# Performance work log

Hardware: AMD Instinct MI355X
Metric: run time of the kernel (lower is better)

Reference implementation:

```python
import jax, jax.numpy as jnp
import numpy as np

K, B, C, T, D, H = 4, 1024, 128, 64, 64, 4  # timeframes, batch, in-feat, seq(=embed!), embed, heads
HD = D // H
EPS = 1e-5


def setup_inputs() -> dict:
    key = jax.random.key(0)
    ks = jax.random.split(key, 8)
    s = lambda k, shape: jax.random.normal(k, shape, dtype=jnp.float32) * 0.05
    return {
        "feats": jax.random.normal(ks[0], (K, B, C, T), dtype=jnp.float32),
        "proj_w": s(ks[1], (K, D, C)),
        "proj_b": jnp.zeros((K, D), jnp.float32),
        "wq": s(ks[2], (K, D, D)),
        "wk": s(ks[3], (K, D, D)),
        "wv": s(ks[4], (K, D, D)),
        "bq": jnp.zeros((K, D), jnp.float32),
        "bk": jnp.zeros((K, D), jnp.float32),
        "bv": jnp.zeros((K, D), jnp.float32),
        "wo": s(ks[5], (K, D, D)),
        "bo": jnp.zeros((K, D), jnp.float32),
        "ng": jnp.ones((K, D), jnp.float32),
        "nb": jnp.zeros((K, D), jnp.float32),
        "tfw": jnp.full((K,), 1.0 / K, jnp.float32),
        "fg": jnp.ones((K * D,), jnp.float32),
        "fb": jnp.zeros((K * D,), jnp.float32),
    }


def _ln(x, g, b):
    m = x.mean(-1, keepdims=True)
    v = ((x - m) ** 2).mean(-1, keepdims=True)
    return (x - m) * jax.lax.rsqrt(v + EPS) * g + b


def reference(feats, proj_w, proj_b, wq, wk, wv, bq, bk, bv, wo, bo, ng, nb, tfw, fg, fb):
    # per-timeframe Linear on channel axis: [K,B,C,T] -> [K,B,D,T]
    proj = jnp.einsum('kbct,kdc->kbdt', feats, proj_w) + proj_b[:, None, :, None]
    ctx4 = jnp.transpose(proj, (1, 0, 2, 3))              # [B,K,D,T] (torch.stack dim=1)
    ctx = ctx4.reshape(B * D, K, T)                       # replicates torch .view(B*T,K,D); needs T==D
    N = B * D
    scale = 1.0 / np.sqrt(HD)
    outs = []
    for i in range(K):  # small fixed loop over K=4 distinct attention blocks
        q_in = ctx[:, i]                                  # [N,D] query = i-th row
        q = (q_in @ wq[i].T + bq[i]).reshape(N, H, HD)
        k = (ctx @ wk[i].T + bk[i]).reshape(N, K, H, HD)
        v = (ctx @ wv[i].T + bv[i]).reshape(N, K, H, HD)
        sc = jnp.einsum('nhe,nkhe->nhk', q, k) * scale    # [N,H,K]
        a = jax.nn.softmax(sc, axis=-1)
        o = jnp.einsum('nhk,nkhe->nhe', a, v).reshape(N, D)
        o = o @ wo[i].T + bo[i]
        outs.append(_ln(o + q_in, ng[i], nb[i]))          # residual + per-tf LayerNorm
    w = jax.nn.softmax(tfw)
    comb = jnp.stack(outs, axis=1) * w[None, :, None]     # [N,K,D] weighted fusion
    fused = comb.reshape(B, D, K * D)                     # torch .view(B,T,K*D)
    return _ln(fused, fg, fb)
```

## Files before the change

kernel.cpp:

```cpp
#include <hip/hip_runtime.h>
#include <math.h>

#define EPSV 1e-5f

typedef __attribute__((ext_vector_type(8))) short short8;
typedef __attribute__((ext_vector_type(4))) float float4v;

__device__ __forceinline__ unsigned short f2bf(float f) {
  unsigned int x = __float_as_uint(f);
  return (unsigned short)((x + 0x7fffu + ((x >> 16) & 1u)) >> 16);
}
__device__ __forceinline__ float bf2f(unsigned short u) {
  return __uint_as_float(((unsigned int)u) << 16);
}
__device__ __forceinline__ float wave_sum64(float v) {
  v += __shfl_xor(v, 1);
  v += __shfl_xor(v, 2);
  v += __shfl_xor(v, 4);
  v += __shfl_xor(v, 8);
  v += __shfl_xor(v, 16);
  v += __shfl_xor(v, 32);
  return v;
}
__device__ __forceinline__ float group16_sum(float v) {
  v += __shfl_xor(v, 1);
  v += __shfl_xor(v, 2);
  v += __shfl_xor(v, 4);
  v += __shfl_xor(v, 8);
  return v;
}

__global__ __launch_bounds__(256, 2) void proj_kernel(
    const float* __restrict__ feats, const float* __restrict__ pw,
    const float* __restrict__ pb, float* __restrict__ ctx) {
  int kb = blockIdx.x;
  int k = kb >> 10;
  int b = kb & 1023;

  __shared__ __align__(16) float F[128 * 64];
  __shared__ float W[64 * 129];

  const float* fsrc = feats + (size_t)kb * 8192;
  const float* wsrc = pw + k * 8192;
  for (int idx = threadIdx.x; idx < 8192; idx += 256) {
    F[idx] = fsrc[idx];
    W[(idx >> 7) * 129 + (idx & 127)] = wsrc[idx];
  }
  __syncthreads();

  int t4 = threadIdx.x & 15;
  int d4 = threadIdx.x >> 4;

  float pb0 = pb[k * 64 + d4 * 4 + 0];
  float pb1 = pb[k * 64 + d4 * 4 + 1];
  float pb2 = pb[k * 64 + d4 * 4 + 2];
  float pb3 = pb[k * 64 + d4 * 4 + 3];

  float acc[4][4];
#pragma unroll
  for (int j = 0; j < 4; ++j) {
    acc[0][j] = pb0; acc[1][j] = pb1; acc[2][j] = pb2; acc[3][j] = pb3;
  }

#pragma unroll 8
  for (int c = 0; c < 128; ++c) {
    float4 f = *(const float4*)&F[c * 64 + t4 * 4];
    float w0 = W[(d4 * 4 + 0) * 129 + c];
    float w1 = W[(d4 * 4 + 1) * 129 + c];
    float w2 = W[(d4 * 4 + 2) * 129 + c];
    float w3 = W[(d4 * 4 + 3) * 129 + c];
    acc[0][0] += w0 * f.x; acc[0][1] += w0 * f.y; acc[0][2] += w0 * f.z; acc[0][3] += w0 * f.w;
    acc[1][0] += w1 * f.x; acc[1][1] += w1 * f.y; acc[1][2] += w1 * f.z; acc[1][3] += w1 * f.w;
    acc[2][0] += w2 * f.x; acc[2][1] += w2 * f.y; acc[2][2] += w2 * f.z; acc[2][3] += w2 * f.w;
    acc[3][0] += w3 * f.x; acc[3][1] += w3 * f.y; acc[3][2] += w3 * f.z; acc[3][3] += w3 * f.w;
  }

  size_t base = ((size_t)b * 64 + k * 16 + d4) * 256 + t4 * 4;
#pragma unroll
  for (int r = 0; r < 4; ++r) {
    float4 o;
    o.x = acc[r][0]; o.y = acc[r][1]; o.z = acc[r][2]; o.w = acc[r][3];
    *(float4*)&ctx[base + r * 64] = o;
  }
}

__global__ __launch_bounds__(256, 2) void attn_fused(
    const float* __restrict__ ctx32,
    const float* __restrict__ wq, const float* __restrict__ wk,
    const float* __restrict__ wv, const float* __restrict__ wo,
    const float* __restrict__ bq, const float* __restrict__ bk,
    const float* __restrict__ bv, const float* __restrict__ bo,
    const float* __restrict__ ng, const float* __restrict__ nb,
    const float* __restrict__ tfw, float* __restrict__ out) {
  __shared__ __align__(16) unsigned short CTP[64 * 264];
  __shared__ __align__(16) unsigned short WBB[4][64 * 72];
  __shared__ __align__(16) unsigned short OSP[4][16 * 72];

  int tid = threadIdx.x;
  int w = tid >> 6, l = tid & 63;
  int l15 = l & 15, lq = l >> 4;

  const float* csrc = ctx32 + (size_t)blockIdx.x * 16384;
  for (int e = tid; e < 16384; e += 256)
    CTP[(e >> 8) * 264 + (e & 255)] = f2bf(csrc[e]);

  float tf0 = tfw[0], tf1 = tfw[1], tf2 = tfw[2], tf3 = tfw[3];
  float tm = fmaxf(fmaxf(tf0, tf1), fmaxf(tf2, tf3));
  float te0 = __expf(tf0 - tm), te1 = __expf(tf1 - tm);
  float te2 = __expf(tf2 - tm), te3 = __expf(tf3 - tm);
  float tden = te0 + te1 + te2 + te3;

  const unsigned short* arow = &CTP[(w * 16 + l15) * 264];
  const float4v zf = {0.0f, 0.0f, 0.0f, 0.0f};

#pragma unroll 1
  for (int i = 0; i < 4; ++i) {
    __syncthreads();
    {
      const float* s0p = wq + i * 4096;
      const float* s1p = wk + i * 4096;
      const float* s2p = wv + i * 4096;
      const float* s3p = wo + i * 4096;
      for (int e = tid; e < 16384; e += 256) {
        int m = e >> 12, d = (e >> 6) & 63, t = e & 63;
        const float* sp = (m == 0) ? s0p : (m == 1) ? s1p : (m == 2) ? s2p : s3p;
        WBB[m][d * 72 + t] = f2bf(sp[d * 64 + t]);
      }
    }
    __syncthreads();

    float wi = ((i == 0) ? te0 : (i == 1) ? te1 : (i == 2) ? te2 : te3) / tden;

    float bqv[4], bkv[4], bvv[4], bov[4], ngv[4], nbv[4];
#pragma unroll
    for (int nt = 0; nt < 4; ++nt) {
      int d = i * 64 + nt * 16 + l15;
      bqv[nt] = bq[d]; bkv[nt] = bk[d]; bvv[nt] = bv[d];
      bov[nt] = bo[d]; ngv[nt] = ng[d]; nbv[nt] = nb[d];
    }

    float4v qacc[4] = {zf, zf, zf, zf};
#pragma unroll
    for (int s = 0; s < 2; ++s) {
      short8 af = *(const short8*)&arow[i * 64 + s * 32 + lq * 8];
#pragma unroll
      for (int nt = 0; nt < 4; ++nt) {
        short8 bf = *(const short8*)&WBB[0][(nt * 16 + l15) * 72 + s * 32 + lq * 8];
        qacc[nt] = __builtin_amdgcn_mfma_f32_16x16x32_bf16(af, bf, qacc[nt], 0, 0, 0);
      }
    }
#pragma unroll
    for (int nt = 0; nt < 4; ++nt)
#pragma unroll
      for (int r = 0; r < 4; ++r) qacc[nt][r] += bqv[nt];

    float4v oacc[4] = {zf, zf, zf, zf};
    float lsum[4][4] = {{0,0,0,0},{0,0,0,0},{0,0,0,0},{0,0,0,0}};

#pragma unroll 1
    for (int j = 0; j < 4; ++j) {
      float4v kacc[4] = {zf, zf, zf, zf};
      float4v vacc[4] = {zf, zf, zf, zf};
#pragma unroll
      for (int s = 0; s < 2; ++s) {
        short8 af = *(const short8*)&arow[j * 64 + s * 32 + lq * 8];
#pragma unroll
        for (int nt = 0; nt < 4; ++nt) {
          short8 bfk = *(const short8*)&WBB[1][(nt * 16 + l15) * 72 + s * 32 + lq * 8];
          short8 bfv = *(const short8*)&WBB[2][(nt * 16 + l15) * 72 + s * 32 + lq * 8];
          kacc[nt] = __builtin_amdgcn_mfma_f32_16x16x32_bf16(af, bfk, kacc[nt], 0, 0, 0);
          vacc[nt] = __builtin_amdgcn_mfma_f32_16x16x32_bf16(af, bfv, vacc[nt], 0, 0, 0);
        }
      }
#pragma unroll
      for (int nt = 0; nt < 4; ++nt)
#pragma unroll
        for (int r = 0; r < 4; ++r) {
          float p = qacc[nt][r] * (kacc[nt][r] + bkv[nt]);
          p = group16_sum(p) * 0.25f;
          float e = __expf(p);
          lsum[nt][r] += e;
          oacc[nt][r] += e * (vacc[nt][r] + bvv[nt]);
        }
    }

#pragma unroll
    for (int nt = 0; nt < 4; ++nt)
#pragma unroll
      for (int r = 0; r < 4; ++r) {
        float ov = oacc[nt][r] / lsum[nt][r];
        OSP[w][(lq * 4 + r) * 72 + nt * 16 + l15] = f2bf(ov);
      }
    __syncthreads();

    float4v o2[4] = {zf, zf, zf, zf};
#pragma unroll
    for (int s = 0; s < 2; ++s) {
      short8 af = *(const short8*)&OSP[w][l15 * 72 + s * 32 + lq * 8];
#pragma unroll
      for (int nt = 0; nt < 4; ++nt) {
        short8 bf = *(const short8*)&WBB[3][(nt * 16 + l15) * 72 + s * 32 + lq * 8];
        o2[nt] = __builtin_amdgcn_mfma_f32_16x16x32_bf16(af, bf, o2[nt], 0, 0, 0);
      }
    }

    float rr[4][4];
#pragma unroll
    for (int nt = 0; nt < 4; ++nt)
#pragma unroll
      for (int r = 0; r < 4; ++r) {
        float qin = bf2f(CTP[(w * 16 + lq * 4 + r) * 264 + i * 64 + nt * 16 + l15]);
        rr[nt][r] = o2[nt][r] + bov[nt] + qin;
      }

#pragma unroll
    for (int r = 0; r < 4; ++r) {
      float sm = group16_sum(rr[0][r] + rr[1][r] + rr[2][r] + rr[3][r]) * (1.0f / 64.0f);
      float vs = 0.0f;
#pragma unroll
      for (int nt = 0; nt < 4; ++nt) { float dx = rr[nt][r] - sm; vs += dx * dx; }
      vs = group16_sum(vs) * (1.0f / 64.0f);
      float inv = rsqrtf(vs + EPSV);
      size_t row = (size_t)blockIdx.x * 64 + w * 16 + lq * 4 + r;
#pragma unroll
      for (int nt = 0; nt < 4; ++nt) {
        float val = wi * ((rr[nt][r] - sm) * inv * ngv[nt] + nbv[nt]);
        out[row * 256 + i * 64 + nt * 16 + l15] = val;
      }
    }
  }
}

__global__ __launch_bounds__(256, 4) void final_ln_kernel(
    float* __restrict__ out, const float* __restrict__ fg,
    const float* __restrict__ fb) {
  int lane = threadIdx.x & 63;
  int wave = threadIdx.x >> 6;
  size_t n = (size_t)blockIdx.x * 4 + wave;

  float4 v = *(const float4*)&out[n * 256 + lane * 4];
  float mean = wave_sum64(v.x + v.y + v.z + v.w) * (1.0f / 256.0f);
  float dx = v.x - mean, dy = v.y - mean, dz = v.z - mean, dw = v.w - mean;
  float var = wave_sum64(dx * dx + dy * dy + dz * dz + dw * dw) * (1.0f / 256.0f);
  float inv = rsqrtf(var + EPSV);

  float4 g = *(const float4*)&fg[lane * 4];
  float4 bb = *(const float4*)&fb[lane * 4];
  float4 o;
  o.x = dx * inv * g.x + bb.x;
  o.y = dy * inv * g.y + bb.y;
  o.z = dz * inv * g.z + bb.z;
  o.w = dw * inv * g.w + bb.w;
  *(float4*)&out[n * 256 + lane * 4] = o;
}

extern "C" void kernel_launch(void* const* d_in, const int* in_sizes, int n_in,
                              void* d_out, int out_size, void* d_ws, size_t ws_size,
                              hipStream_t stream) {
  const float* feats  = (const float*)d_in[0];
  const float* proj_w = (const float*)d_in[1];
  const float* proj_b = (const float*)d_in[2];
  const float* wq  = (const float*)d_in[3];
  const float* wk  = (const float*)d_in[4];
  const float* wv  = (const float*)d_in[5];
  const float* bq  = (const float*)d_in[6];
  const float* bk  = (const float*)d_in[7];
  const float* bv  = (const float*)d_in[8];
  const float* wo  = (const float*)d_in[9];
  const float* bo  = (const float*)d_in[10];
  const float* ng  = (const float*)d_in[11];
  const float* nb  = (const float*)d_in[12];
  const float* tfw = (const float*)d_in[13];
  const float* fg  = (const float*)d_in[14];
  const float* fb  = (const float*)d_in[15];
  float* out = (float*)d_out;
  float* ctx = (float*)d_ws;

  proj_kernel<<<4096, 256, 0, stream>>>(feats, proj_w, proj_b, ctx);
  attn_fused<<<1024, 256, 0, stream>>>(ctx, wq, wk, wv, wo, bq, bk, bv, bo,
                                       ng, nb, tfw, out);
  final_ln_kernel<<<16384, 256, 0, stream>>>(out, fg, fb);
}
```

Baseline: 421.8 us.

## Use split-bf16 MFMA for projection, bf16 ctx, and preconverted weights from global

Adds a prep kernel that converts the projection weights into hi/lo bf16 pairs and converts the attention weights to bf16. The projection now runs on MFMA with three passes (hi*hi, hi*lo, lo*hi) to keep near-fp32 accuracy, and writes its intermediate as bf16, which halves that traffic. The attention kernel now reads weight fragments straight from global or cache instead of staging them in LDS. Block-wide syncs are replaced with per-wave LDS waitcnt fences, which relies on each wave touching only its own LDS rows. The costs are an extra kernel launch and some precision loss in the projection output.

```diff
diff --git a/kernel.cpp b/kernel.cpp
--- a/kernel.cpp
+++ b/kernel.cpp
@@ -29,80 +29,116 @@
   v += __shfl_xor(v, 8);
   return v;
 }
-
-__global__ __launch_bounds__(256, 2) void proj_kernel(
-    const float* __restrict__ feats, const float* __restrict__ pw,
-    const float* __restrict__ pb, float* __restrict__ ctx) {
+__device__ __forceinline__ void lds_fence() {
+  asm volatile("s_waitcnt lgkmcnt(0)" ::: "memory");
+}
+
+__global__ __launch_bounds__(256) void prep_kernel(
+    const float* __restrict__ pw, const float* __restrict__ wq,
+    const float* __restrict__ wk, const float* __restrict__ wv,
+    const float* __restrict__ wo, unsigned short* __restrict__ wph,
+    unsigned short* __restrict__ wpl, unsigned short* __restrict__ wb) {
+  int idx = blockIdx.x * 256 + threadIdx.x;
+  if (idx < 32768) {
+    float f = pw[idx];
+    unsigned short h = f2bf(f);
+    wph[idx] = h;
+    wpl[idx] = f2bf(f - bf2f(h));
+  } else {
+    int e = idx - 32768;
+    int mat = e >> 14, i = (e >> 12) & 3, r = e & 4095;
+    const float* src = (mat == 0) ? wq : (mat == 1) ? wk : (mat == 2) ? wv : wo;
+    wb[((i * 4 + mat) << 12) + r] = f2bf(src[(i << 12) + r]);
+  }
+}
+
+__global__ __launch_bounds__(256, 4) void proj_kernel(
+    const float* __restrict__ feats, const unsigned short* __restrict__ wph,
+    const unsigned short* __restrict__ wpl, const float* __restrict__ pb,
+    unsigned short* __restrict__ ctxbf) {
   int kb = blockIdx.x;
   int k = kb >> 10;
   int b = kb & 1023;
 
-  __shared__ __align__(16) float F[128 * 64];
-  __shared__ float W[64 * 129];
-
+  __shared__ __align__(16) unsigned short FH[64 * 136];
+  __shared__ __align__(16) unsigned short FL[64 * 136];
+
+  int tid = threadIdx.x;
   const float* fsrc = feats + (size_t)kb * 8192;
-  const float* wsrc = pw + k * 8192;
-  for (int idx = threadIdx.x; idx < 8192; idx += 256) {
-    F[idx] = fsrc[idx];
-    W[(idx >> 7) * 129 + (idx & 127)] = wsrc[idx];
+  for (int u = tid; u < 2048; u += 256) {
+    float4 f = *(const float4*)&fsrc[u * 4];
+    int c = u >> 4;
+    int t0 = (u & 15) * 4;
+#pragma unroll
+    for (int q = 0; q < 4; ++q) {
+      float fv = (q == 0) ? f.x : (q == 1) ? f.y : (q == 2) ? f.z : f.w;
+      unsigned short h = f2bf(fv);
+      FH[(t0 + q) * 136 + c] = h;
+      FL[(t0 + q) * 136 + c] = f2bf(fv - bf2f(h));
+    }
   }
   __syncthreads();
 
-  int t4 = threadIdx.x & 15;
-  int d4 = threadIdx.x >> 4;
-
-  float pb0 = pb[k * 64 + d4 * 4 + 0];
-  float pb1 = pb[k * 64 + d4 * 4 + 1];
-  float pb2 = pb[k * 64 + d4 * 4 + 2];
-  float pb3 = pb[k * 64 + d4 * 4 + 3];
-
-  float acc[4][4];
-#pragma unroll
-  for (int j = 0; j < 4; ++j) {
-    acc[0][j] = pb0; acc[1][j] = pb1; acc[2][j] = pb2; acc[3][j] = pb3;
-  }
-
-#pragma unroll 8
-  for (int c = 0; c < 128; ++c) {
-    float4 f = *(const float4*)&F[c * 64 + t4 * 4];
-    float w0 = W[(d4 * 4 + 0) * 129 + c];
-    float w1 = W[(d4 * 4 + 1) * 129 + c];
-    float w2 = W[(d4 * 4 + 2) * 129 + c];
-    float w3 = W[(d4 * 4 + 3) * 129 + c];
-    acc[0][0] += w0 * f.x; acc[0][1] += w0 * f.y; acc[0][2] += w0 * f.z; acc[0][3] += w0 * f.w;
-    acc[1][0] += w1 * f.x; acc[1][1] += w1 * f.y; acc[1][2] += w1 * f.z; acc[1][3] += w1 * f.w;
-    acc[2][0] += w2 * f.x; acc[2][1] += w2 * f.y; acc[2][2] += w2 * f.z; acc[2][3] += w2 * f.w;
-    acc[3][0] += w3 * f.x; acc[3][1] += w3 * f.y; acc[3][2] += w3 * f.z; acc[3][3] += w3 * f.w;
-  }
-
-  size_t base = ((size_t)b * 64 + k * 16 + d4) * 256 + t4 * 4;
-#pragma unroll
-  for (int r = 0; r < 4; ++r) {
-    float4 o;
-    o.x = acc[r][0]; o.y = acc[r][1]; o.z = acc[r][2]; o.w = acc[r][3];
-    *(float4*)&ctx[base + r * 64] = o;
-  }
+  int w = tid >> 6, l = tid & 63;
+  int l15 = l & 15, lq = l >> 4;
+
+  const float4v zf = {0.0f, 0.0f, 0.0f, 0.0f};
+  float4v acc[4] = {zf, zf, zf, zf};
+
+  const unsigned short* whp = wph + k * 8192 + (w * 16 + l15) * 128 + lq * 8;
+  const unsigned short* wlp = wpl + k * 8192 + (w * 16 + l15) * 128 + lq * 8;
+
+#pragma unroll
+  for (int kc = 0; kc < 4; ++kc) {
+    short8 ah = *(const short8*)&whp[kc * 32];
+    short8 al = *(const short8*)&wlp[kc * 32];
+#pragma unroll
+    for (int nt = 0; nt < 4; ++nt) {
+      short8 bh = *(const short8*)&FH[(nt * 16 + l15) * 136 + kc * 32 + lq * 8];
+      short8 bl = *(const short8*)&FL[(nt * 16 + l15) * 136 + kc * 32 + lq * 8];
+      acc[nt] = __builtin_amdgcn_mfma_f32_16x16x32_bf16(ah, bh, acc[nt], 0, 0, 0);
+      acc[nt] = __builtin_amdgcn_mfma_f32_16x16x32_bf16(ah, bl, acc[nt], 0, 0, 0);
+      acc[nt] = __builtin_amdgcn_mfma_f32_16x16x32_bf16(al, bh, acc[nt], 0, 0, 0);
+    }
+  }
+
+  float pbv[4];
+#pragma unroll
+  for (int r = 0; r < 4; ++r) pbv[r] = pb[k * 64 + w * 16 + lq * 4 + r];
+
+  size_t base = ((size_t)b * 64 + k * 16 + w * 4 + lq) * 256;
+#pragma unroll
+  for (int nt = 0; nt < 4; ++nt)
+#pragma unroll
+    for (int r = 0; r < 4; ++r)
+      ctxbf[base + r * 64 + nt * 16 + l15] = f2bf(acc[nt][r] + pbv[r]);
 }
 
 __global__ __launch_bounds__(256, 2) void attn_fused(
-    const float* __restrict__ ctx32,
-    const float* __restrict__ wq, const float* __restrict__ wk,
-    const float* __restrict__ wv, const float* __restrict__ wo,
+    const unsigned short* __restrict__ ctxbf,
+    const unsigned short* __restrict__ wb,
     const float* __restrict__ bq, const float* __restrict__ bk,
     const float* __restrict__ bv, const float* __restrict__ bo,
     const float* __restrict__ ng, const float* __restrict__ nb,
     const float* __restrict__ tfw, float* __restrict__ out) {
   __shared__ __align__(16) unsigned short CTP[64 * 264];
-  __shared__ __align__(16) unsigned short WBB[4][64 * 72];
   __shared__ __align__(16) unsigned short OSP[4][16 * 72];
 
   int tid = threadIdx.x;
   int w = tid >> 6, l = tid & 63;
   int l15 = l & 15, lq = l >> 4;
 
-  const float* csrc = ctx32 + (size_t)blockIdx.x * 16384;
-  for (int e = tid; e < 16384; e += 256)
-    CTP[(e >> 8) * 264 + (e & 255)] = f2bf(csrc[e]);
+  {
+    const unsigned short* csrc = ctxbf + ((size_t)blockIdx.x * 64 + w * 16) * 256;
+#pragma unroll
+    for (int u = 0; u < 8; ++u) {
+      int e = u * 64 + l;
+      int row = e >> 5, c8 = (e & 31) * 8;
+      *(short8*)&CTP[(w * 16 + row) * 264 + c8] =
+          *(const short8*)&csrc[row * 256 + c8];
+    }
+  }
+  lds_fence();
 
   float tf0 = tfw[0], tf1 = tfw[1], tf2 = tfw[2], tf3 = tfw[3];
   float tm = fmaxf(fmaxf(tf0, tf1), fmaxf(tf2, tf3));
@@ -115,28 +151,17 @@
 
 #pragma unroll 1
   for (int i = 0; i < 4; ++i) {
-    __syncthreads();
-    {
-      const float* s0p = wq + i * 4096;
-      const float* s1p = wk + i * 4096;
-      const float* s2p = wv + i * 4096;
-      const float* s3p = wo + i * 4096;
-      for (int e = tid; e < 16384; e += 256) {
-        int m = e >> 12, d = (e >> 6) & 63, t = e & 63;
-        const float* sp = (m == 0) ? s0p : (m == 1) ? s1p : (m == 2) ? s2p : s3p;
-        WBB[m][d * 72 + t] = f2bf(sp[d * 64 + t]);
-      }
-    }
-    __syncthreads();
+#define WFRAG(m, nt, s)                                                        \
+  (*(const short8*)&wb[((i * 4 + (m)) << 12) + ((nt)*16 + l15) * 64 +          \
+                       (s)*32 + lq * 8])
 
     float wi = ((i == 0) ? te0 : (i == 1) ? te1 : (i == 2) ? te2 : te3) / tden;
 
-    float bqv[4], bkv[4], bvv[4], bov[4], ngv[4], nbv[4];
+    float bqv[4], bkv[4], bvv[4];
 #pragma unroll
     for (int nt = 0; nt < 4; ++nt) {
       int d = i * 64 + nt * 16 + l15;
       bqv[nt] = bq[d]; bkv[nt] = bk[d]; bvv[nt] = bv[d];
-      bov[nt] = bo[d]; ngv[nt] = ng[d]; nbv[nt] = nb[d];
     }
 
     float4v qacc[4] = {zf, zf, zf, zf};
@@ -144,15 +169,23 @@
     for (int s = 0; s < 2; ++s) {
       short8 af = *(const short8*)&arow[i * 64 + s * 32 + lq * 8];
 #pragma unroll
+      for (int nt = 0; nt < 4; ++nt)
+        qacc[nt] = __builtin_amdgcn_mfma_f32_16x16x32_bf16(af, WFRAG(0, nt, s),
+                                                           qacc[nt], 0, 0, 0);
+    }
+#pragma unroll
+    for (int nt = 0; nt < 4; ++nt)
+#pragma unroll
+      for (int r = 0; r < 4; ++r) qacc[nt][r] += bqv[nt];
+
+    short8 kf[2][4], vf[2][4];
+#pragma unroll
+    for (int s = 0; s < 2; ++s)
+#pragma unroll
       for (int nt = 0; nt < 4; ++nt) {
-        short8 bf = *(const short8*)&WBB[0][(nt * 16 + l15) * 72 + s * 32 + lq * 8];
-        qacc[nt] = __builtin_amdgcn_mfma_f32_16x16x32_bf16(af, bf, qacc[nt], 0, 0, 0);
+        kf[s][nt] = WFRAG(1, nt, s);
+        vf[s][nt] = WFRAG(2, nt, s);
       }
-    }
-#pragma unroll
-    for (int nt = 0; nt < 4; ++nt)
-#pragma unroll
-      for (int r = 0; r < 4; ++r) qacc[nt][r] += bqv[nt];
 
     float4v oacc[4] = {zf, zf, zf, zf};
     float lsum[4][4] = {{0,0,0,0},{0,0,0,0},{0,0,0,0},{0,0,0,0}};
@@ -166,10 +199,10 @@
         short8 af = *(const short8*)&arow[j * 64 + s * 32 + lq * 8];
 #pragma unroll
         for (int nt = 0; nt < 4; ++nt) {
-          short8 bfk = *(const short8*)&WBB[1][(nt * 16 + l15) * 72 + s * 32 + lq * 8];
-          short8 bfv = *(const short8*)&WBB[2][(nt * 16 + l15) * 72 + s * 32 + lq * 8];
-          kacc[nt] = __builtin_amdgcn_mfma_f32_16x16x32_bf16(af, bfk, kacc[nt], 0, 0, 0);
-          vacc[nt] = __builtin_amdgcn_mfma_f32_16x16x32_bf16(af, bfv, vacc[nt], 0, 0, 0);
+          kacc[nt] = __builtin_amdgcn_mfma_f32_16x16x32_bf16(af, kf[s][nt],
+                                                             kacc[nt], 0, 0, 0);
+          vacc[nt] = __builtin_amdgcn_mfma_f32_16x16x32_bf16(af, vf[s][nt],
+                                                             vacc[nt], 0, 0, 0);
         }
       }
 #pragma unroll
@@ -184,24 +217,29 @@
         }
     }
 
+    lds_fence();
 #pragma unroll
     for (int nt = 0; nt < 4; ++nt)
 #pragma unroll
-      for (int r = 0; r < 4; ++r) {
-        float ov = oacc[nt][r] / lsum[nt][r];
-        OSP[w][(lq * 4 + r) * 72 + nt * 16 + l15] = f2bf(ov);
-      }
-    __syncthreads();
+      for (int r = 0; r < 4; ++r)
+        OSP[w][(lq * 4 + r) * 72 + nt * 16 + l15] = f2bf(oacc[nt][r] / lsum[nt][r]);
+    lds_fence();
 
     float4v o2[4] = {zf, zf, zf, zf};
 #pragma unroll
     for (int s = 0; s < 2; ++s) {
       short8 af = *(const short8*)&OSP[w][l15 * 72 + s * 32 + lq * 8];
 #pragma unroll
-      for (int nt = 0; nt < 4; ++nt) {
-        short8 bf = *(const short8*)&WBB[3][(nt * 16 + l15) * 72 + s * 32 + lq * 8];
-        o2[nt] = __builtin_amdgcn_mfma_f32_16x16x32_bf16(af, bf, o2[nt], 0, 0, 0);
-      }
+      for (int nt = 0; nt < 4; ++nt)
+        o2[nt] = __builtin_amdgcn_mfma_f32_16x16x32_bf16(af, WFRAG(3, nt, s),
+                                                         o2[nt], 0, 0, 0);
+    }
+
+    float bov[4], ngv[4], nbv[4];
+#pragma unroll
+    for (int nt = 0; nt < 4; ++nt) {
+      int d = i * 64 + nt * 16 + l15;
+      bov[nt] = bo[d]; ngv[nt] = ng[d]; nbv[nt] = nb[d];
     }
 
     float rr[4][4];
@@ -228,6 +266,7 @@
         out[row * 256 + i * 64 + nt * 16 + l15] = val;
       }
     }
+#undef WFRAG
   }
 }
 
@@ -274,10 +313,15 @@
   const float* fg  = (const float*)d_in[14];
   const float* fb  = (const float*)d_in[15];
   float* out = (float*)d_out;
-  float* ctx = (float*)d_ws;
-
-  proj_kernel<<<4096, 256, 0, stream>>>(feats, proj_w, proj_b, ctx);
-  attn_fused<<<1024, 256, 0, stream>>>(ctx, wq, wk, wv, wo, bq, bk, bv, bo,
+
+  unsigned short* ctxbf = (unsigned short*)d_ws;
+  unsigned short* wph = (unsigned short*)((char*)d_ws + ((size_t)32 << 20));
+  unsigned short* wpl = wph + 32768;
+  unsigned short* wb  = wpl + 32768;
+
+  prep_kernel<<<384, 256, 0, stream>>>(proj_w, wq, wk, wv, wo, wph, wpl, wb);
+  proj_kernel<<<4096, 256, 0, stream>>>(feats, wph, wpl, proj_b, ctxbf);
+  attn_fused<<<1024, 256, 0, stream>>>(ctxbf, wb, bq, bk, bv, bo,
                                        ng, nb, tfw, out);
   final_ln_kernel<<<16384, 256, 0, stream>>>(out, fg, fb);
 }
```

Measured after the change: 358.1 us. 15.1% less time.
